# Kernel tuning notes

Hardware: AMD Instinct MI355X
Metric: run time of the kernel (lower is better)

The kernel has to match this reference:

```python
import jax, jax.numpy as jnp
import numpy as np

B, T, D_IN, H, D_OUT = 64, 512, 256, 512, 1


def _lstm_layer(x, w_ih, w_hh, b_ih, b_hh):
    """PyTorch-convention LSTM layer. x: [B,T,Din]; w_ih: [4H,Din]; w_hh: [4H,H].
    Gate order: i, f, g, o. Zero initial h/c. Returns [B,T,H]."""
    h_dim = w_hh.shape[1]
    # Precompute input contribution for all timesteps: [B,T,4H]
    xg = jnp.einsum('bti,gi->btg', x, w_ih) + b_ih + b_hh
    xg = jnp.swapaxes(xg, 0, 1)  # [T,B,4H] for scan

    def step(carry, xg_t):
        h, c = carry
        gates = xg_t + h @ w_hh.T  # [B,4H]
        i, f, g, o = jnp.split(gates, 4, axis=-1)
        i = jax.nn.sigmoid(i)
        f = jax.nn.sigmoid(f)
        g = jnp.tanh(g)
        o = jax.nn.sigmoid(o)
        c = f * c + i * g
        h = o * jnp.tanh(c)
        return (h, c), h

    bsz = x.shape[0]
    h0 = jnp.zeros((bsz, h_dim), dtype=x.dtype)
    c0 = jnp.zeros((bsz, h_dim), dtype=x.dtype)
    _, hs = jax.lax.scan(step, (h0, c0), xg)  # hs: [T,B,H]
    return jnp.swapaxes(hs, 0, 1)  # [B,T,H]


def setup_inputs() -> dict:
    key = jax.random.key(0)
    ks = jax.random.split(key, 11)
    s_ih0 = 1.0 / np.sqrt(H)
    inp = {
        'x': jax.random.normal(ks[0], (B, T, D_IN), dtype=jnp.float32),
        'w_ih0': jax.random.uniform(ks[1], (4 * H, D_IN), jnp.float32, -s_ih0, s_ih0),
        'w_hh0': jax.random.uniform(ks[2], (4 * H, H), jnp.float32, -s_ih0, s_ih0),
        'b_ih0': jax.random.uniform(ks[3], (4 * H,), jnp.float32, -s_ih0, s_ih0),
        'b_hh0': jax.random.uniform(ks[4], (4 * H,), jnp.float32, -s_ih0, s_ih0),
        'w_ih1': jax.random.uniform(ks[5], (4 * H, H), jnp.float32, -s_ih0, s_ih0),
        'w_hh1': jax.random.uniform(ks[6], (4 * H, H), jnp.float32, -s_ih0, s_ih0),
        'b_ih1': jax.random.uniform(ks[7], (4 * H,), jnp.float32, -s_ih0, s_ih0),
        'b_hh1': jax.random.uniform(ks[8], (4 * H,), jnp.float32, -s_ih0, s_ih0),
        'w_fc': jax.random.uniform(ks[9], (D_OUT, H), jnp.float32, -s_ih0, s_ih0),
        'b_fc': jax.random.uniform(ks[10], (D_OUT,), jnp.float32, -s_ih0, s_ih0),
    }
    return inp


def reference(x, w_ih0, w_hh0, b_ih0, b_hh0, w_ih1, w_hh1, b_ih1, b_hh1, w_fc, b_fc):
    h = _lstm_layer(x, w_ih0, w_hh0, b_ih0, b_hh0)   # [B,T,H]
    h = _lstm_layer(h, w_ih1, w_hh1, b_ih1, b_hh1)   # [B,T,H]
    last = h[:, -1, :]                               # [B,H]
    logits = last @ w_fc.T + b_fc                    # [B,D_OUT]
    return jax.nn.sigmoid(logits)
```

## Files before the change

### kernel.cpp

```cpp
#include <hip/hip_runtime.h>
#include <stdint.h>
#include <stddef.h>

#define B_ 64
#define T_ 512
#define DIN 256
#define H_ 512
#define NWGF 256

typedef __attribute__((ext_vector_type(8))) short short8;
typedef __attribute__((ext_vector_type(4))) float f32x4;

typedef const __attribute__((address_space(1))) unsigned int* gas_ptr;
typedef __attribute__((address_space(3))) unsigned int* las_ptr;

__device__ __forceinline__ unsigned short f2bf(float f) {
  union { float f; unsigned u; } v; v.f = f;
  return (unsigned short)((v.u + 0x7fffu + ((v.u >> 16) & 1u)) >> 16);
}
__device__ __forceinline__ float bf2f(unsigned short s) {
  union { unsigned u; float f; } v; v.u = ((unsigned)s) << 16; return v.f;
}
__device__ __forceinline__ float sigmoidf_(float x) { return 1.f / (1.f + __expf(-x)); }
__device__ __forceinline__ float tanhf_(float x) { return 1.f - 2.f / (__expf(2.f * x) + 1.f); }

__device__ __forceinline__ void cohstore_u32(unsigned* p, unsigned v) {
  __hip_atomic_store(p, v, __ATOMIC_RELAXED, __HIP_MEMORY_SCOPE_AGENT);
}
__device__ __forceinline__ int cohload_i32(const int* p) {
  return __hip_atomic_load(p, __ATOMIC_RELAXED, __HIP_MEMORY_SCOPE_AGENT);
}
__device__ __forceinline__ void cohstore_i32(int* p, int v) {
  __hip_atomic_store(p, v, __ATOMIC_RELAXED, __HIP_MEMORY_SCOPE_AGENT);
}

__device__ __forceinline__ void gload_lds16(const void* g, void* l) {
  __builtin_amdgcn_global_load_lds((gas_ptr)g, (las_ptr)l, 16, 0, 0);
}

__device__ __forceinline__ void stage_tile_gl(const unsigned short* __restrict__ src,
                                              unsigned short* __restrict__ dst, int tid) {
#pragma unroll
  for (int j = 0; j < 4; ++j) {
    int u = tid + j * 256;
    int g = u >> 4, b = (u & 15) ^ (g & 15);
    gload_lds16(src + (size_t)b * H_ + g * 8,
                dst + (size_t)((tid & ~63) + j * 256) * 8);
  }
}

__global__ void k_convert_x(const float* __restrict__ x, unsigned short* __restrict__ xT) {
  const int nq = T_ * B_ * DIN / 4;
  for (int q = blockIdx.x * blockDim.x + threadIdx.x; q < nq; q += gridDim.x * blockDim.x) {
    int e = q * 4;
    int d = e % DIN;
    int row = e / DIN;
    int b = row & (B_ - 1), t = row / B_;
    float4 v = *(const float4*)(x + ((size_t)b * T_ + t) * DIN + d);
    unsigned short o[4] = { f2bf(v.x), f2bf(v.y), f2bf(v.z), f2bf(v.w) };
    *(uint2*)(xT + (size_t)row * DIN + d) = *(const uint2*)o;
  }
}

__global__ __launch_bounds__(256, 1) void k_lstm10(
    const unsigned short* __restrict__ xT,
    const float* __restrict__ wih0, const float* __restrict__ whh0,
    const float* __restrict__ bih0, const float* __restrict__ bhh0,
    const float* __restrict__ wih1, const float* __restrict__ whh1,
    const float* __restrict__ bih1, const float* __restrict__ bhh1,
    unsigned short* __restrict__ h0, unsigned short* __restrict__ h1,
    int* __restrict__ flg) {
  __shared__ unsigned short hbufA[8192];
  __shared__ unsigned short bufB[8192];
  __shared__ float gbuf[4 * 64 * 5];
  const int bid = blockIdx.x;
  const int grp = bid & 7, cg = bid >> 3;
  const int layer = grp >> 2, bq = grp & 3;
  const int tid = threadIdx.x;
  const int lane = tid & 63, wv = tid >> 6;
  const int l15 = lane & 15, l4 = lane >> 4;
  const int colb = cg * 16, bb = bq * 16;
  const int ucol = tid & 15, ubat = tid >> 4;
  const int lp = (ubat >> 2) * 16 + ucol, ur = ubat & 3;
  int* myflag = flg + (grp * 32 + cg) * 32;
  const int* f_own = flg + (grp * 32) * 32;
  const int* f_l0  = flg + (bq * 32) * 32;

  if (layer == 0) {
    short8 wih[8], whh[16];
    {
      const float* wr = wih0 + (size_t)(wv * H_ + colb + l15) * DIN + l4 * 8;
#pragma unroll
      for (int kk = 0; kk < 8; ++kk) {
        float4 v0 = *(const float4*)(wr + kk * 32);
        float4 v1 = *(const float4*)(wr + kk * 32 + 4);
        unsigned short o[8] = { f2bf(v0.x), f2bf(v0.y), f2bf(v0.z), f2bf(v0.w),
                                f2bf(v1.x), f2bf(v1.y), f2bf(v1.z), f2bf(v1.w) };
        wih[kk] = *(const short8*)o;
      }
      const float* wr2 = whh0 + (size_t)(wv * H_ + colb + l15) * H_ + l4 * 8;
#pragma unroll
      for (int kk = 0; kk < 16; ++kk) {
        float4 v0 = *(const float4*)(wr2 + kk * 32);
        float4 v1 = *(const float4*)(wr2 + kk * 32 + 4);
        unsigned short o[8] = { f2bf(v0.x), f2bf(v0.y), f2bf(v0.z), f2bf(v0.w),
                                f2bf(v1.x), f2bf(v1.y), f2bf(v1.z), f2bf(v1.w) };
        whh[kk] = *(const short8*)o;
      }
    }
    float b0s[4];
#pragma unroll
    for (int s = 0; s < 4; ++s)
      b0s[s] = bih0[s * H_ + colb + ucol] + bhh0[s * H_ + colb + ucol];
    float cst = 0.f;

#pragma unroll
    for (int j = 0; j < 2; ++j) {
      int ch = tid + j * 256;
      int b = ch >> 5, g = ch & 31;
      uint4 v = *(const uint4*)(xT + (size_t)(bb + b) * DIN + g * 8);
      *(uint4*)&bufB[g * 128 + ((b ^ (g & 15)) * 8)] = v;
    }
    __syncthreads();

    for (int t = 0; t < T_; ++t) {
      f32x4 aE = {}, aO = {};
      {
        const unsigned short* xb = bufB + (t & 1) * 4096;
#pragma unroll
        for (int kk = 0; kk < 8; kk += 2) {
          int g0 = kk * 4 + l4, g1 = (kk + 1) * 4 + l4;
          short8 a0 = *(const short8*)&xb[g0 * 128 + ((l15 ^ (g0 & 15)) * 8)];
          short8 a1 = *(const short8*)&xb[g1 * 128 + ((l15 ^ (g1 & 15)) * 8)];
          aE = __builtin_amdgcn_mfma_f32_16x16x32_bf16(a0, wih[kk], aE, 0, 0, 0);
          aO = __builtin_amdgcn_mfma_f32_16x16x32_bf16(a1, wih[kk + 1], aO, 0, 0, 0);
        }
      }
      uint4 xv[2];
      const bool hasx = (t + 1 < T_);
      if (hasx) {
        const unsigned short* xs = xT + (size_t)(t + 1) * (B_ * DIN);
#pragma unroll
        for (int j = 0; j < 2; ++j) {
          int ch = tid + j * 256;
          xv[j] = *(const uint4*)(xs + (size_t)(bb + (ch >> 5)) * DIN + (ch & 31) * 8);
        }
      }
      if (t > 0) {
        for (;;) {
          int v = (lane < 32) ? cohload_i32(f_own + lane * 32) : 0x7fffffff;
          if (__all(v >= t)) break;
        }
        __builtin_amdgcn_sched_barrier(0);
        asm volatile("" ::: "memory");
        stage_tile_gl(h0 + ((size_t)(t - 1) * B_ + bb) * H_, hbufA, tid);
      }
      if (hasx) {
        unsigned short* xd = bufB + ((t + 1) & 1) * 4096;
#pragma unroll
        for (int j = 0; j < 2; ++j) {
          int ch = tid + j * 256;
          int b = ch >> 5, g = ch & 31;
          *(uint4*)&xd[g * 128 + ((b ^ (g & 15)) * 8)] = xv[j];
        }
      }
      __syncthreads();
      if (t > 0) {
#pragma unroll
        for (int kk = 0; kk < 16; kk += 2) {
          int g0 = kk * 4 + l4, g1 = (kk + 1) * 4 + l4;
          short8 a0 = *(const short8*)&hbufA[g0 * 128 + ((l15 ^ (g0 & 15)) * 8)];
          short8 a1 = *(const short8*)&hbufA[g1 * 128 + ((l15 ^ (g1 & 15)) * 8)];
          aE = __builtin_amdgcn_mfma_f32_16x16x32_bf16(a0, whh[kk], aE, 0, 0, 0);
          aO = __builtin_amdgcn_mfma_f32_16x16x32_bf16(a1, whh[kk + 1], aO, 0, 0, 0);
        }
      }
      f32x4 acc = aE + aO;
#pragma unroll
      for (int r = 0; r < 4; ++r) gbuf[(wv * 64 + lane) * 5 + r] = acc[r];
      __syncthreads();
      {
        float g4[4];
#pragma unroll
        for (int s = 0; s < 4; ++s) g4[s] = gbuf[(s * 64 + lp) * 5 + ur] + b0s[s];
        float iv = sigmoidf_(g4[0]), fv = sigmoidf_(g4[1]);
        float gv = tanhf_(g4[2]), ov = sigmoidf_(g4[3]);
        cst = fv * cst + iv * gv;
        unsigned short hv = f2bf(ov * tanhf_(cst));
        unsigned pv = (unsigned)hv | (((unsigned)__shfl_xor((int)hv, 1, 64)) << 16);
        if (!(lane & 1))
          cohstore_u32((unsigned*)(h0 + ((size_t)t * B_ + bb + ubat) * H_ + colb + ucol), pv);
      }
      asm volatile("s_waitcnt vmcnt(0)" ::: "memory");
      __syncthreads();
      if (tid == 0) cohstore_i32(myflag, t + 1);
    }
  } else {
    short8 wA[16], wB[16];
    {
      const float* wrA = wih1 + (size_t)(wv * H_ + colb + l15) * H_ + l4 * 8;
      const float* wrB = whh1 + (size_t)(wv * H_ + colb + l15) * H_ + l4 * 8;
#pragma unroll
      for (int kk = 0; kk < 16; ++kk) {
        float4 a0 = *(const float4*)(wrA + kk * 32);
        float4 a1 = *(const float4*)(wrA + kk * 32 + 4);
        unsigned short oa[8] = { f2bf(a0.x), f2bf(a0.y), f2bf(a0.z), f2bf(a0.w),
                                 f2bf(a1.x), f2bf(a1.y), f2bf(a1.z), f2bf(a1.w) };
        wA[kk] = *(const short8*)oa;
        float4 b0 = *(const float4*)(wrB + kk * 32);
        float4 b1 = *(const float4*)(wrB + kk * 32 + 4);
        unsigned short ob[8] = { f2bf(b0.x), f2bf(b0.y), f2bf(b0.z), f2bf(b0.w),
                                 f2bf(b1.x), f2bf(b1.y), f2bf(b1.z), f2bf(b1.w) };
        wB[kk] = *(const short8*)ob;
      }
    }
    float b1s[4];
#pragma unroll
    for (int s = 0; s < 4; ++s)
      b1s[s] = bih1[s * H_ + colb + ucol] + bhh1[s * H_ + colb + ucol];
    float cst = 0.f;

    for (int t = 0; t < T_; ++t) {
      {
        const int* fp = (lane < 32) ? (f_l0 + lane * 32) : (f_own + (lane - 32) * 32);
        const int need = (lane < 32) ? (t + 1) : t;
        for (;;) {
          int v = cohload_i32(fp);
          if (__all(v >= need)) break;
        }
      }
      __builtin_amdgcn_sched_barrier(0);
      asm volatile("" ::: "memory");
      stage_tile_gl(h0 + ((size_t)t * B_ + bb) * H_, hbufA, tid);
      if (t > 0)
        stage_tile_gl(h1 + ((size_t)(t - 1) * B_ + bb) * H_, bufB, tid);
      __syncthreads();
      f32x4 aE = {}, aO = {}, bE = {}, bO = {};
      if (t > 0) {
#pragma unroll
        for (int kk = 0; kk < 16; kk += 2) {
          int g0 = kk * 4 + l4, g1 = (kk + 1) * 4 + l4;
          int e0 = g0 * 128 + ((l15 ^ (g0 & 15)) * 8);
          int e1 = g1 * 128 + ((l15 ^ (g1 & 15)) * 8);
          aE = __builtin_amdgcn_mfma_f32_16x16x32_bf16(*(const short8*)&hbufA[e0], wA[kk], aE, 0, 0, 0);
          aO = __builtin_amdgcn_mfma_f32_16x16x32_bf16(*(const short8*)&hbufA[e1], wA[kk + 1], aO, 0, 0, 0);
          bE = __builtin_amdgcn_mfma_f32_16x16x32_bf16(*(const short8*)&bufB[e0], wB[kk], bE, 0, 0, 0);
          bO = __builtin_amdgcn_mfma_f32_16x16x32_bf16(*(const short8*)&bufB[e1], wB[kk + 1], bO, 0, 0, 0);
        }
      } else {
#pragma unroll
        for (int kk = 0; kk < 16; kk += 2) {
          int g0 = kk * 4 + l4, g1 = (kk + 1) * 4 + l4;
          int e0 = g0 * 128 + ((l15 ^ (g0 & 15)) * 8);
          int e1 = g1 * 128 + ((l15 ^ (g1 & 15)) * 8);
          aE = __builtin_amdgcn_mfma_f32_16x16x32_bf16(*(const short8*)&hbufA[e0], wA[kk], aE, 0, 0, 0);
          aO = __builtin_amdgcn_mfma_f32_16x16x32_bf16(*(const short8*)&hbufA[e1], wA[kk + 1], aO, 0, 0, 0);
        }
      }
      f32x4 acc = (aE + aO) + (bE + bO);
#pragma unroll
      for (int r = 0; r < 4; ++r) gbuf[(wv * 64 + lane) * 5 + r] = acc[r];
      __syncthreads();
      {
        float g4[4];
#pragma unroll
        for (int s = 0; s < 4; ++s) g4[s] = gbuf[(s * 64 + lp) * 5 + ur] + b1s[s];
        float iv = sigmoidf_(g4[0]), fv = sigmoidf_(g4[1]);
        float gv = tanhf_(g4[2]), ov = sigmoidf_(g4[3]);
        cst = fv * cst + iv * gv;
        unsigned short hv = f2bf(ov * tanhf_(cst));
        unsigned pv = (unsigned)hv | (((unsigned)__shfl_xor((int)hv, 1, 64)) << 16);
        if (!(lane & 1))
          cohstore_u32((unsigned*)(h1 + ((size_t)t * B_ + bb + ubat) * H_ + colb + ucol), pv);
      }
      asm volatile("s_waitcnt vmcnt(0)" ::: "memory");
      __syncthreads();
      if (tid == 0) cohstore_i32(myflag, t + 1);
    }
  }
}

__global__ void k_fc(const unsigned short* __restrict__ h1, const float* __restrict__ w,
                     const float* __restrict__ bfc, float* __restrict__ out) {
  int b = threadIdx.x;
  if (b < B_) {
    const unsigned short* hb = h1 + ((size_t)(T_ - 1) * B_ + b) * H_;
    float s = 0.f;
    for (int j = 0; j < H_; ++j) s += bf2f(hb[j]) * w[j];
    out[b] = sigmoidf_(s + bfc[0]);
  }
}

extern "C" void kernel_launch(void* const* d_in, const int* in_sizes, int n_in,
                              void* d_out, int out_size, void* d_ws, size_t ws_size,
                              hipStream_t stream) {
  (void)in_sizes; (void)n_in; (void)out_size; (void)ws_size;
  const float* x    = (const float*)d_in[0];
  const float* wih0 = (const float*)d_in[1];
  const float* whh0 = (const float*)d_in[2];
  const float* bih0 = (const float*)d_in[3];
  const float* bhh0 = (const float*)d_in[4];
  const float* wih1 = (const float*)d_in[5];
  const float* whh1 = (const float*)d_in[6];
  const float* bih1 = (const float*)d_in[7];
  const float* bhh1 = (const float*)d_in[8];
  const float* wfc  = (const float*)d_in[9];
  const float* bfc  = (const float*)d_in[10];
  float* out = (float*)d_out;

  const size_t HB = (size_t)T_ * B_ * H_ * 2;
  char* ws = (char*)d_ws;
  int* flg = (int*)ws;
  unsigned short* h0 = (unsigned short*)(ws + 32768);
  unsigned short* h1 = (unsigned short*)(ws + 32768 + HB);
  unsigned short* xT = (unsigned short*)(ws + 32768 + 2 * HB);

  hipMemsetAsync(ws, 0, 32768, stream);
  k_convert_x<<<2048, 256, 0, stream>>>(x, xT);
  k_lstm10<<<NWGF, 256, 0, stream>>>(xT, wih0, whh0, bih0, bhh0,
                                     wih1, whh1, bih1, bhh1, h0, h1, flg);
  k_fc<<<1, 64, 0, stream>>>(h1, wfc, bfc, out);
}
```

Measured before the change: 1.731 ms.

## Replace end-of-step barrier with LDS atomic counter and pack step flags contiguously

Drops the trailing __syncthreads before each step's flag publish. Each wave instead increments a shared LDS counter, and the fourth arrival publishes the step flag. gbuf is double-buffered by timestep parity so waves that run ahead cannot overwrite gate values still being read. Flags move from a 128-byte stride to a contiguous layout, so one poll touches fewer cache lines, and layer 0 writes a second mirrored flag copy for layer-1 consumers to spread polling contention. The risks are memory-ordering subtleties across waves and more cross-block traffic for polling, since several flags now share a cache line.

```diff
diff --git a/kernel.cpp b/kernel.cpp
--- a/kernel.cpp
+++ b/kernel.cpp
@@ -62,7 +62,7 @@
   }
 }
 
-__global__ __launch_bounds__(256, 1) void k_lstm10(
+__global__ __launch_bounds__(256, 1) void k_lstm14(
     const unsigned short* __restrict__ xT,
     const float* __restrict__ wih0, const float* __restrict__ whh0,
     const float* __restrict__ bih0, const float* __restrict__ bhh0,
@@ -72,7 +72,8 @@
     int* __restrict__ flg) {
   __shared__ unsigned short hbufA[8192];
   __shared__ unsigned short bufB[8192];
-  __shared__ float gbuf[4 * 64 * 5];
+  __shared__ float gbuf[2][4 * 64 * 5];
+  __shared__ int wcnt;
   const int bid = blockIdx.x;
   const int grp = bid & 7, cg = bid >> 3;
   const int layer = grp >> 2, bq = grp & 3;
@@ -82,9 +83,12 @@
   const int colb = cg * 16, bb = bq * 16;
   const int ucol = tid & 15, ubat = tid >> 4;
   const int lp = (ubat >> 2) * 16 + ucol, ur = ubat & 3;
-  int* myflag = flg + (grp * 32 + cg) * 32;
-  const int* f_own = flg + (grp * 32) * 32;
-  const int* f_l0  = flg + (bq * 32) * 32;
+  int* f_my  = flg + grp * 64 + cg;
+  int* f_myM = flg + (8 + bq) * 64 + cg;
+  const int* f_own = flg + grp * 64;
+  const int* f_l0  = flg + (8 + bq) * 64;
+
+  if (tid == 0) wcnt = 0;
 
   if (layer == 0) {
     short8 wih[8], whh[16];
@@ -148,7 +152,7 @@
       }
       if (t > 0) {
         for (;;) {
-          int v = (lane < 32) ? cohload_i32(f_own + lane * 32) : 0x7fffffff;
+          int v = (lane < 32) ? cohload_i32(f_own + lane) : 0x7fffffff;
           if (__all(v >= t)) break;
         }
         __builtin_amdgcn_sched_barrier(0);
@@ -177,12 +181,12 @@
       }
       f32x4 acc = aE + aO;
 #pragma unroll
-      for (int r = 0; r < 4; ++r) gbuf[(wv * 64 + lane) * 5 + r] = acc[r];
+      for (int r = 0; r < 4; ++r) gbuf[t & 1][(wv * 64 + lane) * 5 + r] = acc[r];
       __syncthreads();
       {
         float g4[4];
 #pragma unroll
-        for (int s = 0; s < 4; ++s) g4[s] = gbuf[(s * 64 + lp) * 5 + ur] + b0s[s];
+        for (int s = 0; s < 4; ++s) g4[s] = gbuf[t & 1][(s * 64 + lp) * 5 + ur] + b0s[s];
         float iv = sigmoidf_(g4[0]), fv = sigmoidf_(g4[1]);
         float gv = tanhf_(g4[2]), ov = sigmoidf_(g4[3]);
         cst = fv * cst + iv * gv;
@@ -192,8 +196,13 @@
           cohstore_u32((unsigned*)(h0 + ((size_t)t * B_ + bb + ubat) * H_ + colb + ucol), pv);
       }
       asm volatile("s_waitcnt vmcnt(0)" ::: "memory");
-      __syncthreads();
-      if (tid == 0) cohstore_i32(myflag, t + 1);
+      if (lane == 0) {
+        int r = atomicAdd(&wcnt, 1);
+        if (r == 4 * t + 3) {
+          cohstore_i32(f_my, t + 1);
+          cohstore_i32(f_myM, t + 1);
+        }
+      }
     }
   } else {
     short8 wA[16], wB[16];
@@ -219,10 +228,11 @@
     for (int s = 0; s < 4; ++s)
       b1s[s] = bih1[s * H_ + colb + ucol] + bhh1[s * H_ + colb + ucol];
     float cst = 0.f;
+    __syncthreads();
 
     for (int t = 0; t < T_; ++t) {
       {
-        const int* fp = (lane < 32) ? (f_l0 + lane * 32) : (f_own + (lane - 32) * 32);
+        const int* fp = (lane < 32) ? (f_l0 + lane) : (f_own + (lane - 32));
         const int need = (lane < 32) ? (t + 1) : t;
         for (;;) {
           int v = cohload_i32(fp);
@@ -259,12 +269,12 @@
       }
       f32x4 acc = (aE + aO) + (bE + bO);
 #pragma unroll
-      for (int r = 0; r < 4; ++r) gbuf[(wv * 64 + lane) * 5 + r] = acc[r];
+      for (int r = 0; r < 4; ++r) gbuf[t & 1][(wv * 64 + lane) * 5 + r] = acc[r];
       __syncthreads();
       {
         float g4[4];
 #pragma unroll
-        for (int s = 0; s < 4; ++s) g4[s] = gbuf[(s * 64 + lp) * 5 + ur] + b1s[s];
+        for (int s = 0; s < 4; ++s) g4[s] = gbuf[t & 1][(s * 64 + lp) * 5 + ur] + b1s[s];
         float iv = sigmoidf_(g4[0]), fv = sigmoidf_(g4[1]);
         float gv = tanhf_(g4[2]), ov = sigmoidf_(g4[3]);
         cst = fv * cst + iv * gv;
@@ -274,8 +284,10 @@
           cohstore_u32((unsigned*)(h1 + ((size_t)t * B_ + bb + ubat) * H_ + colb + ucol), pv);
       }
       asm volatile("s_waitcnt vmcnt(0)" ::: "memory");
-      __syncthreads();
-      if (tid == 0) cohstore_i32(myflag, t + 1);
+      if (lane == 0) {
+        int r = atomicAdd(&wcnt, 1);
+        if (r == 4 * t + 3) cohstore_i32(f_my, t + 1);
+      }
     }
   }
 }
@@ -311,13 +323,13 @@
   const size_t HB = (size_t)T_ * B_ * H_ * 2;
   char* ws = (char*)d_ws;
   int* flg = (int*)ws;
-  unsigned short* h0 = (unsigned short*)(ws + 32768);
-  unsigned short* h1 = (unsigned short*)(ws + 32768 + HB);
-  unsigned short* xT = (unsigned short*)(ws + 32768 + 2 * HB);
-
-  hipMemsetAsync(ws, 0, 32768, stream);
+  unsigned short* h0 = (unsigned short*)(ws + 4096);
+  unsigned short* h1 = (unsigned short*)(ws + 4096 + HB);
+  unsigned short* xT = (unsigned short*)(ws + 4096 + 2 * HB);
+
+  hipMemsetAsync(flg, 0, 4096, stream);
   k_convert_x<<<2048, 256, 0, stream>>>(x, xT);
-  k_lstm10<<<NWGF, 256, 0, stream>>>(xT, wih0, whh0, bih0, bhh0,
+  k_lstm14<<<NWGF, 256, 0, stream>>>(xT, wih0, whh0, bih0, bhh0,
                                      wih1, whh1, bih1, bhh1, h0, h1, flg);
   k_fc<<<1, 64, 0, stream>>>(h1, wfc, bfc, out);
 }
```

Measured after the change: 2.430 ms. 1.4x slower.
